# Performance work log

Measured on AMD Instinct MI355X. Metric: run time of the kernel, lower is better.

## Reference

```python
import jax, jax.numpy as jnp
import numpy as np

D_MODEL = 2048
D_STATE = 64
D_HEAD = 64
N_HEADS = D_MODEL // D_HEAD  # 32
CHUNK = 64
CONV_DIM = D_MODEL + 2 * N_HEADS * D_STATE  # 6144
RMS_EPS = 1.1920929e-07  # torch.finfo(float32).eps (RMSNorm default eps=None)


def setup_inputs() -> dict:
    key = jax.random.key(0)
    ks = jax.random.split(key, 7)
    B, L = 2, 4096
    u = jax.random.normal(ks[0], (B, L, D_MODEL), dtype=jnp.float32)
    out_dim = 2 * D_MODEL + 2 * N_HEADS * D_STATE + N_HEADS  # 8224
    W_in = jax.random.normal(ks[1], (out_dim, D_MODEL), dtype=jnp.float32) * (D_MODEL ** -0.5)
    W_out = jax.random.normal(ks[2], (D_MODEL, D_MODEL), dtype=jnp.float32) * (D_MODEL ** -0.5)
    conv_w = jax.random.normal(ks[3], (CONV_DIM, 1, 3), dtype=jnp.float32) * (3 ** -0.5)
    conv_b = jax.random.normal(ks[4], (CONV_DIM,), dtype=jnp.float32) * 0.1
    # A_log kept negative so per-chunk decay exp(A_log*(chunk-1)) stays bounded
    A_log = -jnp.abs(jax.random.normal(ks[5], (N_HEADS,), dtype=jnp.float32)) * 0.5
    rms_w = jnp.ones((D_MODEL,), dtype=jnp.float32)
    return {"u": u, "W_in": W_in, "W_out": W_out, "conv_w": conv_w,
            "conv_b": conv_b, "A_log": A_log, "rms_w": rms_w}


def _silu(x):
    return x * jax.nn.sigmoid(x)


def _ssd(x, A_log, B_proj, C_proj, chunk):
    # x: [b,L,h,p], B/C: [b,L,h,n] with p == n
    b, L, h, p = x.shape
    n = B_proj.shape[-1]
    c = L // chunk
    xc = x.reshape(b, c, chunk, h, p).transpose(0, 3, 1, 2, 4)       # b h c l p
    Bc = B_proj.reshape(b, c, chunk, h, n).transpose(0, 3, 1, 2, 4)  # b h c l n
    Cc = C_proj.reshape(b, c, chunk, h, n).transpose(0, 3, 1, 2, 4)  # b h c l n
    # A_log is constant over time; full-sequence cumsum then chunked (faithful)
    A_exp = jnp.broadcast_to(A_log[None, :, None], (b, h, L)).astype(jnp.float32)
    A_cum = jnp.cumsum(A_exp, axis=-1).reshape(b, h, c, chunk)
    decay_chunk = jnp.exp(A_cum[..., -1] - A_cum[..., 0])            # b h c
    # Diagonal blocks: quadratic attention inside chunks
    idx = jnp.arange(chunk)
    causal = (idx[:, None] - idx[None, :] >= 0).astype(jnp.float32)  # l x l
    G = jnp.einsum('bhcln,bhcmn->bhclm', Cc, Bc) * causal            # b h c l l
    Y_diag = jnp.einsum('bhclm,bhcmp->bhclp', G, xc)                 # b h c l p
    # Inter-chunk recurrence (note: elementwise product relies on p == n)
    chunk_states = (xc * Bc).sum(axis=3)                             # b h c n
    def step(hstate, inp):
        d, cs = inp
        hstate = hstate * d[..., None] + cs
        return hstate, hstate
    h0 = jnp.zeros((b, h, n), dtype=jnp.float32)
    _, states = jax.lax.scan(step,
                             h0,
                             (decay_chunk.transpose(2, 0, 1),        # c b h
                              chunk_states.transpose(2, 0, 1, 3)))   # c b h n
    prev = jnp.concatenate([jnp.zeros_like(states[:1]), states[:-1]], axis=0)
    prev = prev.transpose(1, 2, 0, 3)                                # b h c n
    # Y_off: [b,h,c,1,n] @ [b,h,c,n,l] -> [b,h,c,l,1], broadcast-added to Y_diag
    Y_off = jnp.einsum('bhcn,bhcln->bhcl', prev, Cc)[..., None]      # b h c l 1
    Y = Y_diag + Y_off                                               # b h c l p
    return Y.transpose(0, 2, 3, 1, 4).reshape(b, L, h, p)


def reference(u, W_in, W_out, conv_w, conv_b, A_log, rms_w):
    B, L, _ = u.shape
    zxbcdt = jnp.einsum('bld,od->blo', u, W_in)
    z = zxbcdt[..., :D_MODEL]
    xBC = zxbcdt[..., D_MODEL:D_MODEL + CONV_DIM]
    # dt = zxbcdt[..., -N_HEADS:]  # computed in original but unused by ssd_step
    xt = xBC.transpose(0, 2, 1)                                      # B C L
    xt = jax.lax.conv_general_dilated(
        xt, conv_w, window_strides=(1,), padding=((1, 1),),
        dimension_numbers=('NCH', 'OIH', 'NCH'),
        feature_group_count=CONV_DIM) + conv_b[None, :, None]
    xBC = _silu(xt).transpose(0, 2, 1)                               # B L C
    x = xBC[..., :D_MODEL].reshape(B, L, N_HEADS, D_HEAD)
    B_proj = xBC[..., D_MODEL:D_MODEL + N_HEADS * D_STATE].reshape(B, L, N_HEADS, D_STATE)
    C_proj = xBC[..., D_MODEL + N_HEADS * D_STATE:].reshape(B, L, N_HEADS, D_STATE)
    y = _ssd(x, A_log, B_proj, C_proj, CHUNK)                        # B L h p
    y = y.reshape(B, L, D_MODEL)
    y = y * _silu(z)
    # RMSNorm with learnable weight
    y = y * jax.lax.rsqrt(jnp.mean(y * y, axis=-1, keepdims=True) + RMS_EPS) * rms_w
    return jnp.einsum('bld,od->blo', y, W_out)
```

## Files before the change

### kernel.cpp

```cpp
#include <hip/hip_runtime.h>
#include <math.h>

#define D_MODEL 2048
#define CONV_DIM 6144
#define N_HEADS 32
#define LSEQ 4096
#define NROWS 8192
#define NCHUNK 64
#define RMS_EPS 1.1920929e-07f

typedef _Float16 half8 __attribute__((ext_vector_type(8)));
typedef float f32x4 __attribute__((ext_vector_type(4)));

__device__ __forceinline__ float silu(float v) { return v / (1.f + expf(-v)); }

__device__ __forceinline__ void glds16(const void* g, void* l) {
    __builtin_amdgcn_global_load_lds((const __attribute__((address_space(1))) void*)g,
                                     (__attribute__((address_space(3))) void*)l,
                                     16, 0, 0);
}

__global__ __launch_bounds__(256) void cvt_f16(
    const float* __restrict__ src, _Float16* __restrict__ dst)
{
    size_t i = ((size_t)blockIdx.x * 256 + threadIdx.x) * 8;
    float4 f0 = *(const float4*)(src + i);
    float4 f1 = *(const float4*)(src + i + 4);
    half8 h;
    h[0] = (_Float16)f0.x; h[1] = (_Float16)f0.y;
    h[2] = (_Float16)f0.z; h[3] = (_Float16)f0.w;
    h[4] = (_Float16)f1.x; h[5] = (_Float16)f1.y;
    h[6] = (_Float16)f1.z; h[7] = (_Float16)f1.w;
    *(half8*)(dst + i) = h;
}

__global__ __launch_bounds__(256) void gemm_f16(
    const _Float16* __restrict__ A, const _Float16* __restrict__ B,
    float* __restrict__ C0, float* __restrict__ C1,
    int M, int N, int K, int nsplit, int ldc0, int ldc1)
{
    __shared__ __align__(16) _Float16 Al[4096];
    __shared__ __align__(16) _Float16 Bl[4096];

    const int tid  = threadIdx.x;
    const int wave = tid >> 6;
    const int lane = tid & 63;
    const int m0 = blockIdx.y * 128;
    const int n0 = blockIdx.x * 128;

    const int s0 = wave * 2, s1 = s0 + 1;
    const int r0 = s0 * 16 + (lane >> 2);
    const int r1 = s1 * 16 + (lane >> 2);
    const int lk0 = ((lane & 3) ^ ((r0 >> 1) & 3)) * 8;
    const int lk1 = ((lane & 3) ^ ((r1 >> 1) & 3)) * 8;
    const _Float16* gA0 = A + (size_t)(m0 + r0) * K + lk0;
    const _Float16* gA1 = A + (size_t)(m0 + r1) * K + lk1;
    const _Float16* gB0 = B + (size_t)(n0 + r0) * K + lk0;
    const _Float16* gB1 = B + (size_t)(n0 + r1) * K + lk1;
    _Float16* lA0 = Al + s0 * 512;
    _Float16* lA1 = Al + s1 * 512;
    _Float16* lB0 = Bl + s0 * 512;
    _Float16* lB1 = Bl + s1 * 512;

    const int wr = (wave >> 1) * 64;
    const int wc = (wave & 1) * 64;
    int offA[4], offB[4];
    #pragma unroll
    for (int t = 0; t < 4; t++) {
        int ra = wr + t * 16 + (lane & 15);
        offA[t] = ra * 64 + ((((lane >> 4) ^ ((ra >> 1) & 3))) << 4);
        int rb = wc + t * 16 + (lane & 15);
        offB[t] = rb * 64 + ((((lane >> 4) ^ ((rb >> 1) & 3))) << 4);
    }

    f32x4 acc[4][4];
    #pragma unroll
    for (int i = 0; i < 4; i++)
        #pragma unroll
        for (int j = 0; j < 4; j++) acc[i][j] = (f32x4)0.f;

    for (int k0 = 0; k0 < K; k0 += 32) {
        __syncthreads();
        glds16(gA0, lA0); glds16(gA1, lA1);
        glds16(gB0, lB0); glds16(gB1, lB1);
        gA0 += 32; gA1 += 32; gB0 += 32; gB1 += 32;
        __syncthreads();

        half8 af[4], bf[4];
        #pragma unroll
        for (int t = 0; t < 4; t++) {
            af[t] = *(const half8*)((const char*)Al + offA[t]);
            bf[t] = *(const half8*)((const char*)Bl + offB[t]);
        }
        #pragma unroll
        for (int mt = 0; mt < 4; mt++)
            #pragma unroll
            for (int nt = 0; nt < 4; nt++)
                acc[mt][nt] = __builtin_amdgcn_mfma_f32_16x16x32_f16(
                    af[mt], bf[nt], acc[mt][nt], 0, 0, 0);
    }

    const int crow = (lane >> 4) * 4;
    const int ccol = lane & 15;
    #pragma unroll
    for (int mt = 0; mt < 4; mt++) {
        #pragma unroll
        for (int nt = 0; nt < 4; nt++) {
            int col = n0 + wc + nt * 16 + ccol;
            int rowb = m0 + wr + mt * 16 + crow;
            #pragma unroll
            for (int j = 0; j < 4; j++) {
                float v = acc[mt][nt][j];
                if (col < nsplit) C0[(size_t)(rowb + j) * ldc0 + col] = v;
                else              C1[(size_t)(rowb + j) * ldc1 + (col - nsplit)] = v;
            }
        }
    }
}

__global__ __launch_bounds__(64) void cs_conv(
    const float* __restrict__ xraw, const float* __restrict__ cw,
    const float* __restrict__ cb, float* __restrict__ cs)
{
    const int CD = CONV_DIM;
    int blk = blockIdx.x;
    int c = blk & 63; int h = (blk >> 6) & 31; int b = blk >> 11;
    int n = threadIdx.x;
    int colx = h * 64 + n;
    int colB = D_MODEL + colx;
    const float* px = xraw + ((size_t)(b * LSEQ + c * 64)) * CD + colx;
    const float* pB = px + D_MODEL;
    float wx0 = cw[colx * 3], wx1 = cw[colx * 3 + 1], wx2 = cw[colx * 3 + 2], bx = cb[colx];
    float wb0 = cw[colB * 3], wb1 = cw[colB * 3 + 1], wb2 = cw[colB * 3 + 2], bb = cb[colB];

    float xm = (c > 0) ? px[-CD] : 0.f;
    float Bm = (c > 0) ? pB[-CD] : 0.f;
    float x0 = px[0], B0 = pB[0];
    float s = 0.f;
    for (int l = 0; l < 64; l++) {
        bool hasp = (c * 64 + l) < (LSEQ - 1);
        float xp = hasp ? px[(size_t)(l + 1) * CD] : 0.f;
        float Bp = hasp ? pB[(size_t)(l + 1) * CD] : 0.f;
        float vx = fmaf(wx0, xm, fmaf(wx1, x0, fmaf(wx2, xp, bx)));
        float vB = fmaf(wb0, Bm, fmaf(wb1, B0, fmaf(wb2, Bp, bb)));
        vx = silu(vx); vB = silu(vB);
        s = fmaf(vx, vB, s);
        xm = x0; x0 = xp; Bm = B0; B0 = Bp;
    }
    cs[(size_t)blk * 64 + n] = s;
}

__global__ void scan_kernel(const float* __restrict__ cs,
                            const float* __restrict__ A_log,
                            float* __restrict__ prev)
{
    int bh = blockIdx.x;
    int h = bh & 31;
    int n = threadIdx.x;
    float d = expf(63.f * A_log[h]);
    float st = 0.f;
    for (int c = 0; c < NCHUNK; c++) {
        size_t i = ((size_t)bh * 64 + c) * 64 + n;
        prev[i] = st;
        st = fmaf(st, d, cs[i]);
    }
}

__global__ __launch_bounds__(256) void ssd_y(
    const float* __restrict__ xraw, const float* __restrict__ cw,
    const float* __restrict__ cb, const float* __restrict__ prev,
    float* __restrict__ yraw)
{
    const int CD = CONV_DIM;
    __shared__ float Cs[64][65];
    __shared__ float Bs[64][65];
    __shared__ float xs[64][64];
    __shared__ float pv[64];
    __shared__ float off[64];
    __shared__ float w0s[192], w1s[192], w2s[192], bss[192];

    int blk = blockIdx.x;
    int c = blk & 63; int h = (blk >> 6) & 31; int b = blk >> 11;
    int tid = threadIdx.x;

    if (tid < 192) {
        int g = tid >> 6, n = tid & 63;
        int col = g * D_MODEL + h * 64 + n;
        w0s[tid] = cw[col * 3]; w1s[tid] = cw[col * 3 + 1]; w2s[tid] = cw[col * 3 + 2];
        bss[tid] = cb[col];
    }
    if (tid < 64) pv[tid] = prev[((size_t)(b * 32 + h) * 64 + c) * 64 + tid];
    __syncthreads();

    size_t rowbase = ((size_t)(b * LSEQ + c * 64)) * CD;
    #pragma unroll
    for (int j = 0; j < 4; j++) {
        int idx = tid + 256 * j;
        int r = idx >> 4;
        int c4 = (idx & 15) * 4;
        bool hasm = (c > 0) || (r > 0);
        bool hasp = (c * 64 + r) < (LSEQ - 1);
        const float* p0 = xraw + rowbase + (size_t)r * CD + h * 64 + c4;
        #pragma unroll
        for (int g = 0; g < 3; g++) {
            const float* pg = p0 + g * D_MODEL;
            float4 rm = hasm ? *(const float4*)(pg - CD) : make_float4(0, 0, 0, 0);
            float4 r0 = *(const float4*)(pg);
            float4 rp = hasp ? *(const float4*)(pg + CD) : make_float4(0, 0, 0, 0);
            int wi = g * 64 + c4;
            float4 o;
            o.x = silu(fmaf(w0s[wi + 0], rm.x, fmaf(w1s[wi + 0], r0.x, fmaf(w2s[wi + 0], rp.x, bss[wi + 0]))));
            o.y = silu(fmaf(w0s[wi + 1], rm.y, fmaf(w1s[wi + 1], r0.y, fmaf(w2s[wi + 1], rp.y, bss[wi + 1]))));
            o.z = silu(fmaf(w0s[wi + 2], rm.z, fmaf(w1s[wi + 2], r0.z, fmaf(w2s[wi + 2], rp.z, bss[wi + 2]))));
            o.w = silu(fmaf(w0s[wi + 3], rm.w, fmaf(w1s[wi + 3], r0.w, fmaf(w2s[wi + 3], rp.w, bss[wi + 3]))));
            if (g == 0)      { *(float4*)&xs[r][c4] = o; }
            else if (g == 1) { Bs[r][c4] = o.x; Bs[r][c4+1] = o.y; Bs[r][c4+2] = o.z; Bs[r][c4+3] = o.w; }
            else             { Cs[r][c4] = o.x; Cs[r][c4+1] = o.y; Cs[r][c4+2] = o.z; Cs[r][c4+3] = o.w; }
        }
    }
    __syncthreads();

    int lb = tid >> 4;
    int mb = tid & 15;
    float g4[4][4];
    #pragma unroll
    for (int i = 0; i < 4; i++)
        #pragma unroll
        for (int j = 0; j < 4; j++) g4[i][j] = 0.f;
    for (int n = 0; n < 64; n++) {
        float cr[4], br[4];
        #pragma unroll
        for (int i = 0; i < 4; i++) cr[i] = Cs[lb * 4 + i][n];
        #pragma unroll
        for (int j = 0; j < 4; j++) br[j] = Bs[mb * 4 + j][n];
        #pragma unroll
        for (int i = 0; i < 4; i++)
            #pragma unroll
            for (int j = 0; j < 4; j++) g4[i][j] = fmaf(cr[i], br[j], g4[i][j]);
    }
    if (tid < 64) {
        float o = 0.f;
        for (int n = 0; n < 64; n++) o = fmaf(pv[n], Cs[tid][n], o);
        off[tid] = o;
    }
    __syncthreads();
    #pragma unroll
    for (int i = 0; i < 4; i++)
        #pragma unroll
        for (int j = 0; j < 4; j++) {
            int l = lb * 4 + i, m = mb * 4 + j;
            Bs[l][m] = (m <= l) ? g4[i][j] : 0.f;
        }
    __syncthreads();

    int l = tid >> 2;
    int pb = (tid & 3) * 16;
    float acc[16];
    float ofl = off[l];
    #pragma unroll
    for (int i = 0; i < 16; i++) acc[i] = ofl;
    int mmax = l | 3;
    for (int m = 0; m <= mmax; m++) {
        float gv = Bs[l][m];
        float4 x0 = *(const float4*)&xs[m][pb];
        float4 x1 = *(const float4*)&xs[m][pb + 4];
        float4 x2 = *(const float4*)&xs[m][pb + 8];
        float4 x3 = *(const float4*)&xs[m][pb + 12];
        acc[0]  = fmaf(gv, x0.x, acc[0]);  acc[1]  = fmaf(gv, x0.y, acc[1]);
        acc[2]  = fmaf(gv, x0.z, acc[2]);  acc[3]  = fmaf(gv, x0.w, acc[3]);
        acc[4]  = fmaf(gv, x1.x, acc[4]);  acc[5]  = fmaf(gv, x1.y, acc[5]);
        acc[6]  = fmaf(gv, x1.z, acc[6]);  acc[7]  = fmaf(gv, x1.w, acc[7]);
        acc[8]  = fmaf(gv, x2.x, acc[8]);  acc[9]  = fmaf(gv, x2.y, acc[9]);
        acc[10] = fmaf(gv, x2.z, acc[10]); acc[11] = fmaf(gv, x2.w, acc[11]);
        acc[12] = fmaf(gv, x3.x, acc[12]); acc[13] = fmaf(gv, x3.y, acc[13]);
        acc[14] = fmaf(gv, x3.z, acc[14]); acc[15] = fmaf(gv, x3.w, acc[15]);
    }
    float* dst = yraw + ((size_t)(b * LSEQ + c * 64 + l)) * D_MODEL + h * 64 + pb;
    #pragma unroll
    for (int q = 0; q < 4; q++)
        *(float4*)(dst + q * 4) = make_float4(acc[q * 4], acc[q * 4 + 1],
                                              acc[q * 4 + 2], acc[q * 4 + 3]);
}

__global__ __launch_bounds__(256) void gate_rms_h(
    const float* __restrict__ ybuf, const float* __restrict__ zbuf,
    const float* __restrict__ rms_w, _Float16* __restrict__ ynh)
{
    int row = blockIdx.x;
    const float* yp = ybuf + (size_t)row * D_MODEL;
    const float* zp = zbuf + (size_t)row * D_MODEL;
    float v[8];
    float ss = 0.f;
    #pragma unroll
    for (int j = 0; j < 8; j++) {
        int col = threadIdx.x + 256 * j;
        float y = yp[col];
        float z = zp[col];
        float gv = y * silu(z);
        v[j] = gv;
        ss = fmaf(gv, gv, ss);
    }
    #pragma unroll
    for (int o = 32; o > 0; o >>= 1) ss += __shfl_xor(ss, o);
    __shared__ float red[4];
    int wid = threadIdx.x >> 6;
    if ((threadIdx.x & 63) == 0) red[wid] = ss;
    __syncthreads();
    float tot = red[0] + red[1] + red[2] + red[3];
    float scale = rsqrtf(tot * (1.f / D_MODEL) + RMS_EPS);
    _Float16* op = ynh + (size_t)row * D_MODEL;
    #pragma unroll
    for (int j = 0; j < 8; j++) {
        int col = threadIdx.x + 256 * j;
        op[col] = (_Float16)(v[j] * scale * rms_w[col]);
    }
}

extern "C" void kernel_launch(void* const* d_in, const int* in_sizes, int n_in,
                              void* d_out, int out_size, void* d_ws, size_t ws_size,
                              hipStream_t stream)
{
    const float* u      = (const float*)d_in[0];
    const float* W_in   = (const float*)d_in[1];
    const float* W_out  = (const float*)d_in[2];
    const float* conv_w = (const float*)d_in[3];
    const float* conv_b = (const float*)d_in[4];
    const float* A_log  = (const float*)d_in[5];
    const float* rms_w  = (const float*)d_in[6];
    float* out = (float*)d_out;

    float* xraw  = (float*)d_ws;
    float* ybuf  = xraw + (size_t)NROWS * CONV_DIM;
    float* csbuf = ybuf + (size_t)NROWS * D_MODEL;
    float* prevb = csbuf + 262144;
    float* zbuf  = out;

    _Float16* uh  = (_Float16*)ybuf;
    _Float16* wh  = uh + (size_t)NROWS * D_MODEL;
    _Float16* woh = (_Float16*)xraw;
    _Float16* ynh = woh + (size_t)D_MODEL * D_MODEL;

    cvt_f16<<<dim3(8192), 256, 0, stream>>>(u, uh);
    cvt_f16<<<dim3(8192), 256, 0, stream>>>(W_in, wh);
    gemm_f16<<<dim3(64, 64), 256, 0, stream>>>(uh, wh, zbuf, xraw,
                                               NROWS, 8192, D_MODEL,
                                               D_MODEL, D_MODEL, CONV_DIM);
    cs_conv<<<dim3(4096), 64, 0, stream>>>(xraw, conv_w, conv_b, csbuf);
    scan_kernel<<<dim3(64), 64, 0, stream>>>(csbuf, A_log, prevb);
    ssd_y<<<dim3(4096), 256, 0, stream>>>(xraw, conv_w, conv_b, prevb, ybuf);
    cvt_f16<<<dim3(2048), 256, 0, stream>>>(W_out, woh);
    gate_rms_h<<<dim3(NROWS), 256, 0, stream>>>(ybuf, zbuf, rms_w, ynh);
    gemm_f16<<<dim3(16, 64), 256, 0, stream>>>(ynh, woh, out, out,
                                               NROWS, D_MODEL, D_MODEL,
                                               D_MODEL, D_MODEL, D_MODEL);
}
```

Before: 845.6 us.

## Replace GEMM with 256x256-tile double-buffered kernel using XCD-aware block swizzle

Both projection GEMMs now use a new kernel with 256x256 output tiles, 512 threads, and a K-tile of 64. Global-to-LDS loads are double-buffered so the next tile streams in while the current one feeds MFMA, with explicit waitcnt and s_setprio around the MFMA groups. The 1D grid is remapped so neighbouring tiles land on the same XCD for L2 reuse. The aim is higher MFMA utilisation and less global traffic per FLOP, at the cost of larger LDS and register use per workgroup (one block per CU) and a hardcoded K of 2048.

```diff
diff --git a/kernel.cpp b/kernel.cpp
--- a/kernel.cpp
+++ b/kernel.cpp
@@ -8,6 +8,9 @@
 #define NROWS 8192
 #define NCHUNK 64
 #define RMS_EPS 1.1920929e-07f
+
+#define GK 2048
+#define KTILES 32
 
 typedef _Float16 half8 __attribute__((ext_vector_type(8)));
 typedef float f32x4 __attribute__((ext_vector_type(4)));
@@ -34,80 +37,137 @@
     *(half8*)(dst + i) = h;
 }
 
-__global__ __launch_bounds__(256) void gemm_f16(
+__global__ __launch_bounds__(512, 1) void gemm_f16_256(
     const _Float16* __restrict__ A, const _Float16* __restrict__ B,
     float* __restrict__ C0, float* __restrict__ C1,
-    int M, int N, int K, int nsplit, int ldc0, int ldc1)
-{
-    __shared__ __align__(16) _Float16 Al[4096];
-    __shared__ __align__(16) _Float16 Bl[4096];
+    int Mtiles, int Ntiles, int nsplit, int ldc0, int ldc1)
+{
+    __shared__ __align__(16) _Float16 Al[2][256 * 64];
+    __shared__ __align__(16) _Float16 Bl[2][256 * 64];
 
     const int tid  = threadIdx.x;
-    const int wave = tid >> 6;
+    const int wid  = tid >> 6;
     const int lane = tid & 63;
-    const int m0 = blockIdx.y * 128;
-    const int n0 = blockIdx.x * 128;
-
-    const int s0 = wave * 2, s1 = s0 + 1;
-    const int r0 = s0 * 16 + (lane >> 2);
-    const int r1 = s1 * 16 + (lane >> 2);
-    const int lk0 = ((lane & 3) ^ ((r0 >> 1) & 3)) * 8;
-    const int lk1 = ((lane & 3) ^ ((r1 >> 1) & 3)) * 8;
-    const _Float16* gA0 = A + (size_t)(m0 + r0) * K + lk0;
-    const _Float16* gA1 = A + (size_t)(m0 + r1) * K + lk1;
-    const _Float16* gB0 = B + (size_t)(n0 + r0) * K + lk0;
-    const _Float16* gB1 = B + (size_t)(n0 + r1) * K + lk1;
-    _Float16* lA0 = Al + s0 * 512;
-    _Float16* lA1 = Al + s1 * 512;
-    _Float16* lB0 = Bl + s0 * 512;
-    _Float16* lB1 = Bl + s1 * 512;
-
-    const int wr = (wave >> 1) * 64;
-    const int wc = (wave & 1) * 64;
-    int offA[4], offB[4];
-    #pragma unroll
-    for (int t = 0; t < 4; t++) {
-        int ra = wr + t * 16 + (lane & 15);
-        offA[t] = ra * 64 + ((((lane >> 4) ^ ((ra >> 1) & 3))) << 4);
-        int rb = wc + t * 16 + (lane & 15);
-        offB[t] = rb * 64 + ((((lane >> 4) ^ ((rb >> 1) & 3))) << 4);
-    }
-
-    f32x4 acc[4][4];
-    #pragma unroll
-    for (int i = 0; i < 4; i++)
+
+    const int nwg = Mtiles * Ntiles;
+    const int cpx = nwg >> 3;
+    const int sw  = (blockIdx.x & 7) * cpx + (blockIdx.x >> 3);
+    const int bm  = sw / Ntiles, bn = sw % Ntiles;
+    const size_t m0 = (size_t)bm * 256, n0 = (size_t)bn * 256;
+
+    const int srow = tid >> 3;
+    const int sk16 = (tid & 7) ^ (srow & 7);
+    const _Float16* gA = A + (m0 + srow) * GK + sk16 * 8;
+    const _Float16* gB = B + (n0 + srow) * GK + sk16 * 8;
+
+    const int wm = wid >> 2, wn = wid & 3;
+    const int rowA = (wm * 128 + (lane & 15)) * 128;
+    const int rowB = (wn * 64 + (lane & 15)) * 128;
+    const int slotx0 = (((0 * 4 + (lane >> 4)) ^ (lane & 7)) << 4);
+    const int slotx1 = (((1 * 4 + (lane >> 4)) ^ (lane & 7)) << 4);
+
+    f32x4 acc[8][4];
+    #pragma unroll
+    for (int i = 0; i < 8; i++)
         #pragma unroll
         for (int j = 0; j < 4; j++) acc[i][j] = (f32x4)0.f;
-
-    for (int k0 = 0; k0 < K; k0 += 32) {
-        __syncthreads();
-        glds16(gA0, lA0); glds16(gA1, lA1);
-        glds16(gB0, lB0); glds16(gB1, lB1);
-        gA0 += 32; gA1 += 32; gB0 += 32; gB1 += 32;
-        __syncthreads();
-
-        half8 af[4], bf[4];
-        #pragma unroll
-        for (int t = 0; t < 4; t++) {
-            af[t] = *(const half8*)((const char*)Al + offA[t]);
-            bf[t] = *(const half8*)((const char*)Bl + offB[t]);
-        }
-        #pragma unroll
-        for (int mt = 0; mt < 4; mt++)
-            #pragma unroll
-            for (int nt = 0; nt < 4; nt++)
-                acc[mt][nt] = __builtin_amdgcn_mfma_f32_16x16x32_f16(
-                    af[mt], bf[nt], acc[mt][nt], 0, 0, 0);
+    half8 bf0, bf1, bf2, bf3;
+
+#define STAGE(bufsel, tt) do {                                              \
+    const _Float16* _ga = gA + (size_t)(tt) * 64;                           \
+    const _Float16* _gb = gB + (size_t)(tt) * 64;                           \
+    char* _la = (char*)&Al[(bufsel)][0] + wid * 1024;                       \
+    char* _lb = (char*)&Bl[(bufsel)][0] + wid * 1024;                       \
+    glds16(_ga,               _la);                                         \
+    glds16(_ga + 1 * 64 * GK, _la + 1 * 8192);                              \
+    glds16(_ga + 2 * 64 * GK, _la + 2 * 8192);                              \
+    glds16(_ga + 3 * 64 * GK, _la + 3 * 8192);                              \
+    glds16(_gb,               _lb);                                         \
+    glds16(_gb + 1 * 64 * GK, _lb + 1 * 8192);                              \
+    glds16(_gb + 2 * 64 * GK, _lb + 2 * 8192);                              \
+    glds16(_gb + 3 * 64 * GK, _lb + 3 * 8192);                              \
+} while (0)
+
+#define MFMA16(mh)                                                          \
+    __builtin_amdgcn_s_setprio(1);                                          \
+    acc[(mh)*4+0][0] = __builtin_amdgcn_mfma_f32_16x16x32_f16(af0, bf0, acc[(mh)*4+0][0], 0, 0, 0); \
+    acc[(mh)*4+0][1] = __builtin_amdgcn_mfma_f32_16x16x32_f16(af0, bf1, acc[(mh)*4+0][1], 0, 0, 0); \
+    acc[(mh)*4+0][2] = __builtin_amdgcn_mfma_f32_16x16x32_f16(af0, bf2, acc[(mh)*4+0][2], 0, 0, 0); \
+    acc[(mh)*4+0][3] = __builtin_amdgcn_mfma_f32_16x16x32_f16(af0, bf3, acc[(mh)*4+0][3], 0, 0, 0); \
+    acc[(mh)*4+1][0] = __builtin_amdgcn_mfma_f32_16x16x32_f16(af1, bf0, acc[(mh)*4+1][0], 0, 0, 0); \
+    acc[(mh)*4+1][1] = __builtin_amdgcn_mfma_f32_16x16x32_f16(af1, bf1, acc[(mh)*4+1][1], 0, 0, 0); \
+    acc[(mh)*4+1][2] = __builtin_amdgcn_mfma_f32_16x16x32_f16(af1, bf2, acc[(mh)*4+1][2], 0, 0, 0); \
+    acc[(mh)*4+1][3] = __builtin_amdgcn_mfma_f32_16x16x32_f16(af1, bf3, acc[(mh)*4+1][3], 0, 0, 0); \
+    acc[(mh)*4+2][0] = __builtin_amdgcn_mfma_f32_16x16x32_f16(af2, bf0, acc[(mh)*4+2][0], 0, 0, 0); \
+    acc[(mh)*4+2][1] = __builtin_amdgcn_mfma_f32_16x16x32_f16(af2, bf1, acc[(mh)*4+2][1], 0, 0, 0); \
+    acc[(mh)*4+2][2] = __builtin_amdgcn_mfma_f32_16x16x32_f16(af2, bf2, acc[(mh)*4+2][2], 0, 0, 0); \
+    acc[(mh)*4+2][3] = __builtin_amdgcn_mfma_f32_16x16x32_f16(af2, bf3, acc[(mh)*4+2][3], 0, 0, 0); \
+    acc[(mh)*4+3][0] = __builtin_amdgcn_mfma_f32_16x16x32_f16(af3, bf0, acc[(mh)*4+3][0], 0, 0, 0); \
+    acc[(mh)*4+3][1] = __builtin_amdgcn_mfma_f32_16x16x32_f16(af3, bf1, acc[(mh)*4+3][1], 0, 0, 0); \
+    acc[(mh)*4+3][2] = __builtin_amdgcn_mfma_f32_16x16x32_f16(af3, bf2, acc[(mh)*4+3][2], 0, 0, 0); \
+    acc[(mh)*4+3][3] = __builtin_amdgcn_mfma_f32_16x16x32_f16(af3, bf3, acc[(mh)*4+3][3], 0, 0, 0); \
+    __builtin_amdgcn_s_setprio(0);
+
+#define LOADA(bufsel, mh, SLX)                                              \
+    half8 af0 = *(const half8*)((const char*)&Al[(bufsel)][0] + rowA + ((mh)*64+ 0)*128 + (SLX)); \
+    half8 af1 = *(const half8*)((const char*)&Al[(bufsel)][0] + rowA + ((mh)*64+16)*128 + (SLX)); \
+    half8 af2 = *(const half8*)((const char*)&Al[(bufsel)][0] + rowA + ((mh)*64+32)*128 + (SLX)); \
+    half8 af3 = *(const half8*)((const char*)&Al[(bufsel)][0] + rowA + ((mh)*64+48)*128 + (SLX));
+
+#define LOADB(bufsel, SLX)                                                  \
+    bf0 = *(const half8*)((const char*)&Bl[(bufsel)][0] + rowB +    0 + (SLX)); \
+    bf1 = *(const half8*)((const char*)&Bl[(bufsel)][0] + rowB + 2048 + (SLX)); \
+    bf2 = *(const half8*)((const char*)&Bl[(bufsel)][0] + rowB + 4096 + (SLX)); \
+    bf3 = *(const half8*)((const char*)&Bl[(bufsel)][0] + rowB + 6144 + (SLX));
+
+    STAGE(0, 0);
+
+    for (int t = 0; t < KTILES; ++t) {
+        const int cur = t & 1;
+        if (t + 1 < KTILES) {
+            STAGE(cur ^ 1, t + 1);
+            __builtin_amdgcn_sched_barrier(0);
+            asm volatile("s_waitcnt vmcnt(8)" ::: "memory");
+        } else {
+            asm volatile("s_waitcnt vmcnt(0)" ::: "memory");
+        }
+        __builtin_amdgcn_sched_barrier(0);
+        __builtin_amdgcn_s_barrier();
+        {
+            LOADA(cur, 0, slotx0)
+            LOADB(cur, slotx0)
+            MFMA16(0)
+            __builtin_amdgcn_s_barrier();
+        }
+        {
+            LOADA(cur, 1, slotx0)
+            __builtin_amdgcn_s_barrier();
+            MFMA16(1)
+            __builtin_amdgcn_s_barrier();
+        }
+        {
+            LOADA(cur, 0, slotx1)
+            LOADB(cur, slotx1)
+            __builtin_amdgcn_s_barrier();
+            MFMA16(0)
+            __builtin_amdgcn_s_barrier();
+        }
+        {
+            LOADA(cur, 1, slotx1)
+            __builtin_amdgcn_s_barrier();
+            MFMA16(1)
+            __builtin_amdgcn_s_barrier();
+        }
     }
 
     const int crow = (lane >> 4) * 4;
     const int ccol = lane & 15;
     #pragma unroll
-    for (int mt = 0; mt < 4; mt++) {
+    for (int mt = 0; mt < 8; mt++) {
         #pragma unroll
         for (int nt = 0; nt < 4; nt++) {
-            int col = n0 + wc + nt * 16 + ccol;
-            int rowb = m0 + wr + mt * 16 + crow;
+            int col  = (int)n0 + wn * 64 + nt * 16 + ccol;
+            int rowb = (int)m0 + wm * 128 + mt * 16 + crow;
             #pragma unroll
             for (int j = 0; j < 4; j++) {
                 float v = acc[mt][nt][j];
@@ -116,6 +176,10 @@
             }
         }
     }
+#undef STAGE
+#undef MFMA16
+#undef LOADA
+#undef LOADB
 }
 
 __global__ __launch_bounds__(64) void cs_conv(
@@ -342,15 +406,13 @@
 
     cvt_f16<<<dim3(8192), 256, 0, stream>>>(u, uh);
     cvt_f16<<<dim3(8192), 256, 0, stream>>>(W_in, wh);
-    gemm_f16<<<dim3(64, 64), 256, 0, stream>>>(uh, wh, zbuf, xraw,
-                                               NROWS, 8192, D_MODEL,
-                                               D_MODEL, D_MODEL, CONV_DIM);
+    gemm_f16_256<<<dim3(1024), 512, 0, stream>>>(uh, wh, zbuf, xraw,
+                                                 32, 32, D_MODEL, D_MODEL, CONV_DIM);
     cs_conv<<<dim3(4096), 64, 0, stream>>>(xraw, conv_w, conv_b, csbuf);
     scan_kernel<<<dim3(64), 64, 0, stream>>>(csbuf, A_log, prevb);
     ssd_y<<<dim3(4096), 256, 0, stream>>>(xraw, conv_w, conv_b, prevb, ybuf);
     cvt_f16<<<dim3(2048), 256, 0, stream>>>(W_out, woh);
     gate_rms_h<<<dim3(NROWS), 256, 0, stream>>>(ybuf, zbuf, rms_w, ynh);
-    gemm_f16<<<dim3(16, 64), 256, 0, stream>>>(ynh, woh, out, out,
-                                               NROWS, D_MODEL, D_MODEL,
-                                               D_MODEL, D_MODEL, D_MODEL);
-}
+    gemm_f16_256<<<dim3(256), 512, 0, stream>>>(ynh, woh, out, out,
+                                                32, 8, D_MODEL, D_MODEL, D_MODEL);
+}
```

New measurement: 777.6 us. 1.09x faster.
